# Optimization experiments

Measured on AMD Instinct MI355X. Metric: run time of the kernel, lower is better.

## Reference

```python
import jax, jax.numpy as jnp
import numpy as np

B, L, N_EMBD = 4, 2048, 768
N_HIDDEN, N_BINS, V, VOCAB = 32, 8, 64, 1270
TIME_BINS = np.array([0.0, 0.25, 0.5, 1.0, 2.0, 5.0, 10.0, 20.0, 40.0], dtype=np.float32)
TASK_TOKENS = np.arange(5, 5 + 19 * V, 19, dtype=np.int32)  # sorted, all > 0, < VOCAB


def setup_inputs() -> dict:
    key = jax.random.key(0)
    k0, k1, k2, k3, k4, k5 = jax.random.split(key, 6)
    # ages in years, sorted along trajectory; next-event age is slightly later
    age = jnp.sort(jax.random.uniform(k0, (B, L), dtype=jnp.float32) * 80.0, axis=-1)
    targets_age = age + jax.random.uniform(k1, (B, L), dtype=jnp.float32) * 5.0
    targets = jax.random.randint(k2, (B, L), 0, VOCAB, dtype=jnp.int32)
    h = jax.random.normal(k3, (B, L, N_EMBD), dtype=jnp.float32)
    # nn.Linear weights (stored transposed so forward is x @ W)
    W1 = jax.random.normal(k4, (N_EMBD, N_BINS * N_HIDDEN), dtype=jnp.float32) * 0.02
    W2 = jax.random.normal(k5, (N_HIDDEN, V), dtype=jnp.float32) * 0.02
    task_tokens = jnp.asarray(TASK_TOKENS)
    time_bins = jnp.asarray(TIME_BINS)
    return {"h": h, "age": age, "targets_age": targets_age, "targets": targets,
            "W1": W1, "W2": W2, "task_tokens": task_tokens, "time_bins": time_bins}


def reference(h, age, targets_age, targets, W1, W2, task_tokens, time_bins):
    # ---- time_to_event ----
    # delta_t[b, j, k] = targets_age[b, k] - age[b, j]
    delta_t = targets_age[:, None, :] - age[:, :, None]  # (B, L, L)
    # triu token map: keep target token at column k if k >= j, else 0
    jj = jnp.arange(L, dtype=jnp.int32)
    triu_mask = jj[None, :] >= jj[:, None]  # (L, L)
    targets_exp = jnp.where(triu_mask[None], targets[:, None, :], 0)  # (B, L, L)
    # token_map: task token t -> rank+1 in sorted task tokens; others -> 0
    tmap = jnp.zeros((VOCAB,), dtype=jnp.int32).at[task_tokens].set(
        jnp.arange(1, V + 1, dtype=jnp.int32))
    mapped = tmap[targets_exp]  # (B, L, L) values in [0, V]
    # scatter_reduce(amin): for each (b, j, v) find min column k with mapped == v
    seg_base = (jnp.arange(B * L, dtype=jnp.int32) * (V + 1)).reshape(B, L, 1)
    seg_ids = (seg_base + mapped).reshape(-1)
    k_idx = jnp.broadcast_to(jj[None, None, :], (B, L, L)).reshape(-1)
    tok = jax.ops.segment_min(k_idx, seg_ids, num_segments=B * L * (V + 1))
    tok = tok.reshape(B, L, V + 1)[:, :, 1:]  # drop bucket 0 -> (B, L, V)
    no_event = tok >= L  # empty segments fill with int max
    tok = jnp.minimum(tok, L - 1)
    tte = jnp.take_along_axis(delta_t, tok, axis=-1)  # (B, L, V)
    # ---- piecewise_time ----
    last_censor = targets_age[:, -1:] - age  # (B, L)
    starts, ends = time_bins[:-1], time_bins[1:]  # (N_BINS,)
    tte_e = tte[:, :, None, :]  # (B, L, 1, V)
    occur = (tte_e > starts[:, None]) & (tte_e <= ends[:, None]) & (~no_event[:, :, None, :])
    cens = jnp.clip(last_censor[:, :, None, None], 0.0, (ends - starts)[:, None])
    surv_or_event_time = jnp.where(occur, tte_e, cens)  # (B, L, N_BINS, V)
    # ---- head ----
    hh = (h @ W1).reshape(B, L, N_BINS, N_HIDDEN)
    log_lambda = jnp.einsum('blnh,hv->blnv', hh, W2)  # (B, L, N_BINS, V)
    # ---- loss ----
    ll_survival = jnp.mean(-jnp.exp(log_lambda) * surv_or_event_time)
    ll_to_event = jnp.mean(log_lambda * occur.astype(log_lambda.dtype))
    return -(ll_survival + ll_to_event)
```

## Files before the change

### kernel.cpp

```cpp
#include <hip/hip_runtime.h>
#include <hip/hip_bf16.h>

#define B_      4
#define L_      2048
#define NE_     768
#define NOUT_   256
#define NH_     32
#define NB_     8
#define V_      64
#define VOCAB_  1270
#define NC_     32
#define CS_     64
#define BM_     32
#define BK_     32
#define NROWS_  8192
#define GRID_MAIN_ (NROWS_ / BM_)
#define INV_M_  (1.0f / 4194304.0f)
#define INF_    0x7FFFFFFF

typedef float f32x4 __attribute__((ext_vector_type(4)));
typedef short s16x8 __attribute__((ext_vector_type(8)));

__device__ __forceinline__ unsigned short f2bf(float x) {
    union { float f; unsigned u; } c; c.f = x;
    unsigned u = c.u;
    return (unsigned short)((u + 0x7fffu + ((u >> 16) & 1u)) >> 16);
}


__global__ void __launch_bounds__(256)
k_pre(const int* __restrict__ task_tokens, const float* __restrict__ W1,
      const float* __restrict__ W2,
      int* __restrict__ tmap, short* __restrict__ W1t, short* __restrict__ W2t) {
    const int tid = threadIdx.x;
    if (blockIdx.x == 0) {
        for (int t = tid; t < VOCAB_; t += 256) tmap[t] = 0;
        __syncthreads();
        if (tid < V_) tmap[task_tokens[tid]] = tid + 1;
        for (int i = tid; i < V_ * NH_; i += 256) {
            int col = i >> 5, j = i & 31;
            W2t[col * NH_ + j] = (short)f2bf(W2[j * V_ + col]);
        }
        return;
    }
    __shared__ float tl[64][67];
    const int tIdx = blockIdx.x - 1;
    const int kt = (tIdx % 12) * 64;
    const int ct = (tIdx / 12) * 64;
    #pragma unroll
    for (int p = 0; p < 4; ++p) {
        int kk = (tid >> 4) + p * 16;
        int cc = (tid & 15) * 4;
        float4 v = *reinterpret_cast<const float4*>(&W1[(kt + kk) * NOUT_ + ct + cc]);
        tl[kk][cc] = v.x; tl[kk][cc + 1] = v.y; tl[kk][cc + 2] = v.z; tl[kk][cc + 3] = v.w;
    }
    __syncthreads();
    #pragma unroll
    for (int p = 0; p < 8; ++p) {
        int oc  = (tid >> 5) + p * 8;
        int ok2 = (tid & 31) * 2;
        unsigned pk = ((unsigned)f2bf(tl[ok2 + 1][oc]) << 16) | f2bf(tl[ok2][oc]);
        *reinterpret_cast<unsigned*>(&W1t[(ct + oc) * NE_ + kt + ok2]) = pk;
    }
}

__global__ void __launch_bounds__(64)
k_occ(const int* __restrict__ targets, const int* __restrict__ tmap,
      int* __restrict__ mt, int* __restrict__ firstocc) {
    __shared__ int smt[CS_];
    const int b = blockIdx.x >> 5, c = blockIdx.x & 31;
    const int v = threadIdx.x;
    int tgt = targets[b * L_ + c * CS_ + v];
    int mval = tmap[tgt] - 1;
    mt[b * L_ + c * CS_ + v] = mval;
    smt[v] = mval;
    __syncthreads();
    int first = INF_;
    for (int j = CS_ - 1; j >= 0; --j)
        if (smt[j] == v) first = c * CS_ + j;
    firstocc[(b * NC_ + c) * V_ + v] = first;
}

__global__ void __launch_bounds__(512)
k_main(const float* __restrict__ h, const float* __restrict__ age,
       const float* __restrict__ targets_age,
       const int* __restrict__ mt, const int* __restrict__ firstocc,
       const short* __restrict__ W1t, const short* __restrict__ W2t,
       const float* __restrict__ time_bins, float* __restrict__ partials) {
    __shared__ __align__(16) short sA[2][BM_][40];
    __shared__ __align__(16) short sB[2][256][40];
    __shared__ __align__(16) short sH[NB_][BM_][40];
    __shared__ __align__(16) short sW2[V_][40];
    __shared__ float stte[BM_][66];
    __shared__ int   smt[CS_];
    __shared__ float sage[BM_];
    __shared__ float sred[8];

    const int tid = threadIdx.x;
    const int w   = tid >> 6;
    const int l   = tid & 63;
    const int l15 = l & 15;
    const int l4  = l >> 4;
    const int r0  = blockIdx.x * BM_;
    const int b   = r0 >> 11;
    const int pos0 = r0 & (L_ - 1);
    const int c    = pos0 >> 6;
    const int off  = pos0 - c * CS_;

    const int arow = tid >> 4;
    const int akc  = tid & 15;
    const int brow = tid >> 2;
    const int bch  = tid & 3;
    const float* hA  = &h[(r0 + arow) * NE_ + akc * 2];
    const short* bS0 = &W1t[brow * NE_ + bch * 8];
    const short* bS1 = &W1t[(brow + 128) * NE_ + bch * 8];
    float2 aReg = *(const float2*)hA;
    s16x8  bReg0 = *(const s16x8*)bS0;
    s16x8  bReg1 = *(const s16x8*)bS1;

    if (tid < CS_)  smt[tid]  = mt[b * L_ + c * CS_ + tid];
    if (tid < BM_)  sage[tid] = age[r0 + tid];
    if (tid < 256) {
        int col = tid >> 2, ch = tid & 3;
        *(s16x8*)&sW2[col][ch * 8] = *(const s16x8*)&W2t[col * NH_ + ch * 8];
    }
    __syncthreads();

    {
        const int v  = tid & 63;
        const int rg = tid >> 6;
        int cur = INF_;
        for (int cc = c + 1; cc < NC_; ++cc)
            cur = min(cur, firstocc[(b * NC_ + cc) * V_ + v]);
        int* stteI = (int*)stte;
        const int jmin = off + rg * 4;
        for (int j = CS_ - 1; j >= jmin; --j) {
            if (smt[j] == v) cur = c * CS_ + j;
            int br = j - off;
            if ((br >> 2) == rg) stteI[br * 66 + v] = cur;
        }
        #pragma unroll
        for (int jr = 0; jr < 4; ++jr) {
            int br  = rg * 4 + jr;
            int tok = stteI[br * 66 + v];
            float val = -1.0f;
            if (tok != INF_) val = targets_age[b * L_ + tok] - sage[br];
            stte[br][v] = val;
        }
    }

    f32x4 acc[2][2] = {};
    {
        unsigned pk = ((unsigned)f2bf(aReg.y) << 16) | f2bf(aReg.x);
        *(unsigned*)&sA[0][arow][akc * 2] = pk;
        *(s16x8*)&sB[0][brow][bch * 8]       = bReg0;
        *(s16x8*)&sB[0][brow + 128][bch * 8] = bReg1;
    }
    __syncthreads();

    for (int t = 0; t < NE_ / BK_; ++t) {
        const int cur = t & 1;
        if (t < NE_ / BK_ - 1) {
            int kn = (t + 1) * BK_;
            aReg  = *(const float2*)(hA + kn);
            bReg0 = *(const s16x8*)(bS0 + kn);
            bReg1 = *(const s16x8*)(bS1 + kn);
        }
        s16x8 af0 = *(const s16x8*)&sA[cur][l15][l4 * 8];
        s16x8 af1 = *(const s16x8*)&sA[cur][16 + l15][l4 * 8];
        s16x8 bf0 = *(const s16x8*)&sB[cur][w * 32 + l15][l4 * 8];
        s16x8 bf1 = *(const s16x8*)&sB[cur][w * 32 + 16 + l15][l4 * 8];
        acc[0][0] = __builtin_amdgcn_mfma_f32_16x16x32_bf16(af0, bf0, acc[0][0], 0, 0, 0);
        acc[0][1] = __builtin_amdgcn_mfma_f32_16x16x32_bf16(af0, bf1, acc[0][1], 0, 0, 0);
        acc[1][0] = __builtin_amdgcn_mfma_f32_16x16x32_bf16(af1, bf0, acc[1][0], 0, 0, 0);
        acc[1][1] = __builtin_amdgcn_mfma_f32_16x16x32_bf16(af1, bf1, acc[1][1], 0, 0, 0);
        if (t < NE_ / BK_ - 1) {
            unsigned pk = ((unsigned)f2bf(aReg.y) << 16) | f2bf(aReg.x);
            *(unsigned*)&sA[cur ^ 1][arow][akc * 2] = pk;
            *(s16x8*)&sB[cur ^ 1][brow][bch * 8]       = bReg0;
            *(s16x8*)&sB[cur ^ 1][brow + 128][bch * 8] = bReg1;
        }
        __syncthreads();
    }

    #pragma unroll
    for (int rf = 0; rf < 2; ++rf)
        #pragma unroll
        for (int cfg = 0; cfg < 2; ++cfg) {
            int jj = cfg * 16 + l15;
            #pragma unroll
            for (int jr = 0; jr < 4; ++jr)
                sH[w][rf * 16 + l4 * 4 + jr][jj] = (short)f2bf(acc[rf][cfg][jr]);
        }
    __syncthreads();

    const int rf = w & 1;
    const int cf = w >> 1;
    const int v  = cf * 16 + l15;
    s16x8 b2 = *(const s16x8*)&sW2[v][l4 * 8];

    float tb[NB_ + 1];
    #pragma unroll
    for (int n = 0; n <= NB_; ++n) tb[n] = time_bins[n];

    float tva[4], lcv[4];
    const float lastTA = targets_age[b * L_ + (L_ - 1)];
    #pragma unroll
    for (int jr = 0; jr < 4; ++jr) {
        int br = rf * 16 + l4 * 4 + jr;
        tva[jr] = stte[br][v];
        lcv[jr] = lastTA - sage[br];
    }

    float part = 0.0f;
    const f32x4 zero = {};
    #pragma unroll
    for (int n = 0; n < NB_; ++n) {
        s16x8 a2 = *(const s16x8*)&sH[n][rf * 16 + l15][l4 * 8];
        f32x4 c2 = __builtin_amdgcn_mfma_f32_16x16x32_bf16(a2, b2, zero, 0, 0, 0);
        float sn = tb[n], en = tb[n + 1], wn = en - sn;
        #pragma unroll
        for (int jr = 0; jr < 4; ++jr) {
            float ll = c2[jr];
            float ex = __expf(ll);
            float cn = fminf(fmaxf(lcv[jr], 0.0f), wn);
            float tv = tva[jr];
            bool occ = (tv > sn) && (tv <= en);
            part += cn * ex + (occ ? ex * (tv - cn) - ll : 0.0f);
        }
    }

    #pragma unroll
    for (int offs = 32; offs > 0; offs >>= 1) part += __shfl_xor(part, offs);
    if (l == 0) sred[w] = part;
    __syncthreads();
    if (tid == 0) {
        float s = 0.0f;
        #pragma unroll
        for (int i = 0; i < 8; ++i) s += sred[i];
        partials[blockIdx.x] = s;
    }
}

__global__ void k_final(const float* __restrict__ partials, float* __restrict__ out) {
    __shared__ float sred[4];
    float x = partials[threadIdx.x];
    #pragma unroll
    for (int off = 32; off > 0; off >>= 1) x += __shfl_xor(x, off);
    if ((threadIdx.x & 63) == 0) sred[threadIdx.x >> 6] = x;
    __syncthreads();
    if (threadIdx.x == 0)
        out[0] = (sred[0] + sred[1] + sred[2] + sred[3]) * INV_M_;
}

extern "C" void kernel_launch(void* const* d_in, const int* in_sizes, int n_in,
                              void* d_out, int out_size, void* d_ws, size_t ws_size,
                              hipStream_t stream) {
    const float* h           = (const float*)d_in[0];
    const float* age         = (const float*)d_in[1];
    const float* targets_age = (const float*)d_in[2];
    const int*   targets     = (const int*)d_in[3];
    const float* W1          = (const float*)d_in[4];
    const float* W2          = (const float*)d_in[5];
    const int*   task_tokens = (const int*)d_in[6];
    const float* time_bins   = (const float*)d_in[7];
    float* out = (float*)d_out;

    char* ws = (char*)d_ws;
    int*   tmap     = (int*)(ws + 0);
    int*   mt       = (int*)(ws + 8192);
    int*   firstocc = (int*)(ws + 40960);
    short* W1t      = (short*)(ws + 73728);
    short* W2t      = (short*)(ws + 466944);
    float* partials = (float*)(ws + 471040);

    hipLaunchKernelGGL(k_pre, dim3(49), dim3(256), 0, stream,
                       task_tokens, W1, W2, tmap, W1t, W2t);
    hipLaunchKernelGGL(k_occ, dim3(B_ * NC_), dim3(64), 0, stream,
                       targets, tmap, mt, firstocc);
    hipLaunchKernelGGL(k_main, dim3(GRID_MAIN_), dim3(512), 0, stream,
                       h, age, targets_age, mt, firstocc, W1t, W2t, time_bins, partials);
    hipLaunchKernelGGL(k_final, dim3(1), dim3(256), 0, stream, partials, out);
}
```

Before: 38.34 us.

## Merge prep kernels and fold final reduction into main via last-block atomic

Combines the W1/W2 transpose, token mapping and first-occurrence kernels into one prep launch by replacing the tmap table with a linear search over task tokens in shared memory. It also folds the final reduction into k_main with a last-block atomic counter. This cuts the pipeline from four launches to two. The cross-chunk firstocc min scan is now split across all 8 waves with a shared-memory reduction, and the loss expression is simplified slightly. The trade-offs are an extra atomic per block and a 64-iteration compare loop per target.

New measurement: 37.46 us. 2.3% less time.

```diff
diff --git a/kernel.cpp b/kernel.cpp
--- a/kernel.cpp
+++ b/kernel.cpp
@@ -14,7 +14,7 @@
 #define BM_     32
 #define BK_     32
 #define NROWS_  8192
-#define GRID_MAIN_ (NROWS_ / BM_)
+#define GRID_MAIN_ 256
 #define INV_M_  (1.0f / 4194304.0f)
 #define INF_    0x7FFFFFFF
 
@@ -29,55 +29,62 @@
 
 
 __global__ void __launch_bounds__(256)
-k_pre(const int* __restrict__ task_tokens, const float* __restrict__ W1,
-      const float* __restrict__ W2,
-      int* __restrict__ tmap, short* __restrict__ W1t, short* __restrict__ W2t) {
+k_prep(const int* __restrict__ task_tokens, const float* __restrict__ W1,
+       const float* __restrict__ W2, const int* __restrict__ targets,
+       short* __restrict__ W1t, short* __restrict__ W2t,
+       int* __restrict__ mt, int* __restrict__ firstocc, unsigned* __restrict__ cnt) {
+    __shared__ float tl[64][67];
+    __shared__ int   stask[V_];
+    __shared__ int   smt[4][CS_];
     const int tid = threadIdx.x;
-    if (blockIdx.x == 0) {
-        for (int t = tid; t < VOCAB_; t += 256) tmap[t] = 0;
+
+    if (blockIdx.x < 48) {
+        const int tIdx = blockIdx.x;
+        const int kt = (tIdx % 12) * 64;
+        const int ct = (tIdx / 12) * 64;
+        #pragma unroll
+        for (int p = 0; p < 4; ++p) {
+            int kk = (tid >> 4) + p * 16;
+            int cc = (tid & 15) * 4;
+            float4 v = *reinterpret_cast<const float4*>(&W1[(kt + kk) * NOUT_ + ct + cc]);
+            tl[kk][cc] = v.x; tl[kk][cc + 1] = v.y; tl[kk][cc + 2] = v.z; tl[kk][cc + 3] = v.w;
+        }
         __syncthreads();
-        if (tid < V_) tmap[task_tokens[tid]] = tid + 1;
-        for (int i = tid; i < V_ * NH_; i += 256) {
+        #pragma unroll
+        for (int p = 0; p < 8; ++p) {
+            int oc  = (tid >> 5) + p * 8;
+            int ok2 = (tid & 31) * 2;
+            unsigned pk = ((unsigned)f2bf(tl[ok2 + 1][oc]) << 16) | f2bf(tl[ok2][oc]);
+            *reinterpret_cast<unsigned*>(&W1t[(ct + oc) * NE_ + kt + ok2]) = pk;
+        }
+        return;
+    }
+    if (blockIdx.x == 48) {
+        if (tid == 0) cnt[0] = 0u;
+        #pragma unroll
+        for (int q = 0; q < 8; ++q) {
+            int i = tid + q * 256;
             int col = i >> 5, j = i & 31;
             W2t[col * NH_ + j] = (short)f2bf(W2[j * V_ + col]);
         }
         return;
     }
-    __shared__ float tl[64][67];
-    const int tIdx = blockIdx.x - 1;
-    const int kt = (tIdx % 12) * 64;
-    const int ct = (tIdx / 12) * 64;
-    #pragma unroll
-    for (int p = 0; p < 4; ++p) {
-        int kk = (tid >> 4) + p * 16;
-        int cc = (tid & 15) * 4;
-        float4 v = *reinterpret_cast<const float4*>(&W1[(kt + kk) * NOUT_ + ct + cc]);
-        tl[kk][cc] = v.x; tl[kk][cc + 1] = v.y; tl[kk][cc + 2] = v.z; tl[kk][cc + 3] = v.w;
-    }
-    __syncthreads();
-    #pragma unroll
-    for (int p = 0; p < 8; ++p) {
-        int oc  = (tid >> 5) + p * 8;
-        int ok2 = (tid & 31) * 2;
-        unsigned pk = ((unsigned)f2bf(tl[ok2 + 1][oc]) << 16) | f2bf(tl[ok2][oc]);
-        *reinterpret_cast<unsigned*>(&W1t[(ct + oc) * NE_ + kt + ok2]) = pk;
-    }
-}
-
-__global__ void __launch_bounds__(64)
-k_occ(const int* __restrict__ targets, const int* __restrict__ tmap,
-      int* __restrict__ mt, int* __restrict__ firstocc) {
-    __shared__ int smt[CS_];
-    const int b = blockIdx.x >> 5, c = blockIdx.x & 31;
-    const int v = threadIdx.x;
-    int tgt = targets[b * L_ + c * CS_ + v];
-    int mval = tmap[tgt] - 1;
+    if (tid < V_) stask[tid] = task_tokens[tid];
+    __syncthreads();
+    const int gi = tid >> 6;
+    const int v  = tid & 63;
+    const int g  = (blockIdx.x - 49) * 4 + gi;
+    const int b  = g >> 5, c = g & 31;
+    int t = targets[b * L_ + c * CS_ + v];
+    int mval = -1;
+    #pragma unroll
+    for (int j = 0; j < V_; ++j)
+        mval = (stask[j] == t) ? j : mval;
     mt[b * L_ + c * CS_ + v] = mval;
-    smt[v] = mval;
-    __syncthreads();
+    smt[gi][v] = mval;
     int first = INF_;
     for (int j = CS_ - 1; j >= 0; --j)
-        if (smt[j] == v) first = c * CS_ + j;
+        if (smt[gi][j] == v) first = c * CS_ + j;
     firstocc[(b * NC_ + c) * V_ + v] = first;
 }
 
@@ -86,15 +93,19 @@
        const float* __restrict__ targets_age,
        const int* __restrict__ mt, const int* __restrict__ firstocc,
        const short* __restrict__ W1t, const short* __restrict__ W2t,
-       const float* __restrict__ time_bins, float* __restrict__ partials) {
+       const float* __restrict__ time_bins, float* __restrict__ partials,
+       unsigned* __restrict__ cnt, float* __restrict__ out) {
     __shared__ __align__(16) short sA[2][BM_][40];
     __shared__ __align__(16) short sB[2][256][40];
     __shared__ __align__(16) short sH[NB_][BM_][40];
     __shared__ __align__(16) short sW2[V_][40];
     __shared__ float stte[BM_][66];
+    __shared__ int   sminI[8][V_];
     __shared__ int   smt[CS_];
     __shared__ float sage[BM_];
     __shared__ float sred[8];
+    __shared__ float s2[4];
+    __shared__ int   sLast;
 
     const int tid = threadIdx.x;
     const int w   = tid >> 6;
@@ -124,14 +135,24 @@
         int col = tid >> 2, ch = tid & 3;
         *(s16x8*)&sW2[col][ch * 8] = *(const s16x8*)&W2t[col * NH_ + ch * 8];
     }
-    __syncthreads();
 
     {
-        const int v  = tid & 63;
-        const int rg = tid >> 6;
         int cur = INF_;
-        for (int cc = c + 1; cc < NC_; ++cc)
-            cur = min(cur, firstocc[(b * NC_ + cc) * V_ + v]);
+        #pragma unroll
+        for (int k = 0; k < 4; ++k) {
+            int cc = c + 1 + w + k * 8;
+            if (cc < NC_) cur = min(cur, firstocc[(b * NC_ + cc) * V_ + l]);
+        }
+        sminI[w][l] = cur;
+    }
+    __syncthreads();
+
+    {
+        const int v  = l;
+        const int rg = w;
+        int cur = INF_;
+        #pragma unroll
+        for (int ww = 0; ww < 8; ++ww) cur = min(cur, sminI[ww][v]);
         int* stteI = (int*)stte;
         const int jmin = off + rg * 4;
         for (int j = CS_ - 1; j >= jmin; --j) {
@@ -223,10 +244,10 @@
         for (int jr = 0; jr < 4; ++jr) {
             float ll = c2[jr];
             float ex = __expf(ll);
-            float cn = fminf(fmaxf(lcv[jr], 0.0f), wn);
             float tv = tva[jr];
             bool occ = (tv > sn) && (tv <= en);
-            part += cn * ex + (occ ? ex * (tv - cn) - ll : 0.0f);
+            float cn = fminf(fmaxf(lcv[jr], 0.0f), wn);
+            part += ex * (occ ? tv : cn) - (occ ? ll : 0.0f);
         }
     }
 
@@ -238,19 +259,21 @@
         float s = 0.0f;
         #pragma unroll
         for (int i = 0; i < 8; ++i) s += sred[i];
-        partials[blockIdx.x] = s;
-    }
-}
-
-__global__ void k_final(const float* __restrict__ partials, float* __restrict__ out) {
-    __shared__ float sred[4];
-    float x = partials[threadIdx.x];
-    #pragma unroll
-    for (int off = 32; off > 0; off >>= 1) x += __shfl_xor(x, off);
-    if ((threadIdx.x & 63) == 0) sred[threadIdx.x >> 6] = x;
-    __syncthreads();
-    if (threadIdx.x == 0)
-        out[0] = (sred[0] + sred[1] + sred[2] + sred[3]) * INV_M_;
+        __hip_atomic_store(&partials[blockIdx.x], s, __ATOMIC_RELEASE, __HIP_MEMORY_SCOPE_AGENT);
+        unsigned old = __hip_atomic_fetch_add(cnt, 1u, __ATOMIC_ACQ_REL, __HIP_MEMORY_SCOPE_AGENT);
+        sLast = (old == GRID_MAIN_ - 1u);
+    }
+    __syncthreads();
+    if (sLast) {
+        float x = 0.0f;
+        if (tid < 256)
+            x = __hip_atomic_load(&partials[tid], __ATOMIC_RELAXED, __HIP_MEMORY_SCOPE_AGENT);
+        #pragma unroll
+        for (int o = 32; o > 0; o >>= 1) x += __shfl_xor(x, o);
+        if (tid < 256 && (tid & 63) == 0) s2[tid >> 6] = x;
+        __syncthreads();
+        if (tid == 0) out[0] = (s2[0] + s2[1] + s2[2] + s2[3]) * INV_M_;
+    }
 }
 
 extern "C" void kernel_launch(void* const* d_in, const int* in_sizes, int n_in,
@@ -267,18 +290,16 @@
     float* out = (float*)d_out;
 
     char* ws = (char*)d_ws;
-    int*   tmap     = (int*)(ws + 0);
-    int*   mt       = (int*)(ws + 8192);
-    int*   firstocc = (int*)(ws + 40960);
-    short* W1t      = (short*)(ws + 73728);
-    short* W2t      = (short*)(ws + 466944);
-    float* partials = (float*)(ws + 471040);
-
-    hipLaunchKernelGGL(k_pre, dim3(49), dim3(256), 0, stream,
-                       task_tokens, W1, W2, tmap, W1t, W2t);
-    hipLaunchKernelGGL(k_occ, dim3(B_ * NC_), dim3(64), 0, stream,
-                       targets, tmap, mt, firstocc);
+    int*      mt       = (int*)(ws + 0);
+    int*      firstocc = (int*)(ws + 32768);
+    short*    W1t      = (short*)(ws + 65536);
+    short*    W2t      = (short*)(ws + 458752);
+    float*    partials = (float*)(ws + 462848);
+    unsigned* cnt      = (unsigned*)(ws + 463872);
+
+    hipLaunchKernelGGL(k_prep, dim3(81), dim3(256), 0, stream,
+                       task_tokens, W1, W2, targets, W1t, W2t, mt, firstocc, cnt);
     hipLaunchKernelGGL(k_main, dim3(GRID_MAIN_), dim3(512), 0, stream,
-                       h, age, targets_age, mt, firstocc, W1t, W2t, time_bins, partials);
-    hipLaunchKernelGGL(k_final, dim3(1), dim3(256), 0, stream, partials, out);
+                       h, age, targets_age, mt, firstocc, W1t, W2t, time_bins,
+                       partials, cnt, out);
 }
```
